# Kernel tuning notes

Measured on AMD Instinct MI355X. Metric: run time of the kernel, lower is better.

The kernel has to match this reference:

```python
import jax, jax.numpy as jnp
import numpy as np

N = 131072
L_ENC = 100
L_DEC = 50
H = 200            # decoder_hidden_dim
SPD = L_ENC + 2 * (L_ENC // 2 + 1)  # 202, signal + amplitudes + phases


def _lin(k, out_d, in_d):
    kw, kb = jax.random.split(k)
    lim = 1.0 / np.sqrt(in_d)
    w = jax.random.uniform(kw, (out_d, in_d), jnp.float32, -lim, lim)
    b = jax.random.uniform(kb, (out_d,), jnp.float32, -lim, lim)
    return w, b


def setup_inputs() -> dict:
    key = jax.random.key(0)
    ks = jax.random.split(key, 16)
    enc_w1, enc_b1 = _lin(ks[0], 100, SPD)
    enc_w2, enc_b2 = _lin(ks[1], SPD, 100)
    enc_wl, enc_bl = _lin(ks[2], H, SPD)
    lim = 1.0 / np.sqrt(H)
    w_ih = jax.random.uniform(ks[3], (3 * H, 1), jnp.float32, -lim, lim)
    w_hh = jax.random.uniform(ks[4], (3 * H, H), jnp.float32, -lim, lim)
    b_ih = jax.random.uniform(ks[5], (3 * H,), jnp.float32, -lim, lim)
    b_hh = jax.random.uniform(ks[6], (3 * H,), jnp.float32, -lim, lim)
    dec_w1, dec_b1 = _lin(ks[7], H // 2, H)
    dec_w2, dec_b2 = _lin(ks[8], H // 4, H // 2)
    dec_w3, dec_b3 = _lin(ks[9], 1, H // 4)
    encoder_input = jax.random.normal(ks[10], (N, L_ENC, 1), jnp.float32)
    return dict(encoder_input=encoder_input,
                enc_w1=enc_w1, enc_b1=enc_b1, enc_w2=enc_w2, enc_b2=enc_b2,
                enc_wl=enc_wl, enc_bl=enc_bl,
                w_ih=w_ih, w_hh=w_hh, b_ih=b_ih, b_hh=b_hh,
                dec_w1=dec_w1, dec_b1=dec_b1, dec_w2=dec_w2, dec_b2=dec_b2,
                dec_w3=dec_w3, dec_b3=dec_b3)


def _lrelu(x):
    return jax.nn.leaky_relu(x, negative_slope=0.01)


def reference(encoder_input, enc_w1, enc_b1, enc_w2, enc_b2, enc_wl, enc_bl,
              w_ih, w_hh, b_ih, b_hh,
              dec_w1, dec_b1, dec_w2, dec_b2, dec_w3, dec_b3):
    # --- MLPEncoder: rfft features + 3-layer MLP ---
    f = jnp.fft.rfft(encoder_input, axis=1, norm='forward')  # [N, 51, 1] complex
    sig = jnp.concatenate([encoder_input, jnp.abs(f), jnp.angle(f)], axis=1)[..., 0]  # [N, 202]
    x = _lrelu(sig @ enc_w1.T + enc_b1)
    x = _lrelu(x @ enc_w2.T + enc_b2)
    h0 = x @ enc_wl.T + enc_bl  # [N, H]

    dec_in0 = encoder_input[:, -1, :]  # [N, 1]

    def step(carry, _):
        h, dec_in = carry
        gx = dec_in @ w_ih.T + b_ih       # [N, 3H]
        gh = h @ w_hh.T + b_hh            # [N, 3H]
        xr, xz, xn = jnp.split(gx, 3, axis=-1)
        hr, hz, hn = jnp.split(gh, 3, axis=-1)
        r = jax.nn.sigmoid(xr + hr)
        z = jax.nn.sigmoid(xz + hz)
        n = jnp.tanh(xn + r * hn)
        h_new = (1.0 - z) * n + z * h
        y = _lrelu(h_new @ dec_w1.T + dec_b1)
        y = _lrelu(y @ dec_w2.T + dec_b2)
        y = y @ dec_w3.T + dec_b3         # [N, 1]
        return (h_new, jax.lax.stop_gradient(y)), y

    _, ys = jax.lax.scan(step, (h0, dec_in0), None, length=L_DEC)  # [L_DEC, N, 1]
    return jnp.transpose(ys, (1, 0, 2))  # [N, L_DEC, 1]
```

## Files before the change

kernel.cpp:

```cpp
#include <hip/hip_runtime.h>
#include <math.h>

typedef _Float16 half8  __attribute__((ext_vector_type(8)));
typedef float    floatx4 __attribute__((ext_vector_type(4)));

#define MFMA16(a, b, c) __builtin_amdgcn_mfma_f32_16x16x32_f16((a), (b), (c), 0, 0, 0)

constexpr unsigned WJT_OFF  = 0;
constexpr unsigned WD1_OFF  = 292864;
constexpr unsigned W2_OFF   = 350208;
constexpr unsigned WE1_OFF  = 366592;
constexpr unsigned WE2_OFF  = 416768;
constexpr unsigned WEL_OFF  = 470016;
constexpr unsigned WIHC_OFF = 563200;
constexpr unsigned BSUM_OFF = 565696;
constexpr unsigned BHHN_OFF = 568192;
constexpr unsigned B1P_OFF  = 569024;
constexpr unsigned B2P_OFF  = 569472;
constexpr unsigned W3P_OFF  = 569728;
constexpr unsigned BE1_OFF  = 569984;
constexpr unsigned BE2_OFF  = 570432;
constexpr unsigned BEL_OFF  = 571264;
constexpr unsigned B3_OFF   = 572096;
constexpr unsigned CT_OFF   = 572112;
constexpr unsigned WS_NEED  = 573712;

constexpr unsigned BST_OFF   = 106496;
constexpr unsigned W2L_OFF   = 129024;
constexpr unsigned CHK_OFF   = 146432;
constexpr unsigned DECIN_OFF = 162816;
constexpr unsigned SMEM_BYTES = 163840;

__device__ __forceinline__ half8 lds_frag16(const _Float16* p) {
  union { uint4 u; half8 h; } cv;
  cv.u = *(const uint4*)p;
  return cv.h;
}
__device__ __forceinline__ half8 g_frag(const _Float16* p) {
  union { uint4 u; half8 h; } cv;
  cv.u = *(const uint4*)p;
  return cv.h;
}
__device__ __forceinline__ void gload_lds16(const _Float16* gsrc, _Float16* lds) {
  __builtin_amdgcn_global_load_lds(
      (const __attribute__((address_space(1))) unsigned int*)gsrc,
      (__attribute__((address_space(3))) unsigned int*)lds, 16, 0, 0);
}
__device__ __forceinline__ float sigm(float x) {
  return __builtin_amdgcn_rcpf(1.f + __builtin_amdgcn_exp2f(-1.44269504f * x));
}
__device__ __forceinline__ float tanh_(float x) {
  return 1.f - 2.f * __builtin_amdgcn_rcpf(1.f + __builtin_amdgcn_exp2f(2.88539008f * x));
}
__device__ __forceinline__ int chk_idx(int row, int col) {
  return (row * 32 + col) ^ (((row >> 1) & 3) << 3);
}

__global__ __launch_bounds__(256) void prep_kernel(
    const float* __restrict__ enc_w1, const float* __restrict__ enc_b1,
    const float* __restrict__ enc_w2, const float* __restrict__ enc_b2,
    const float* __restrict__ enc_wl, const float* __restrict__ enc_bl,
    const float* __restrict__ w_ih,  const float* __restrict__ w_hh,
    const float* __restrict__ b_ih,  const float* __restrict__ b_hh,
    const float* __restrict__ dw1, const float* __restrict__ db1,
    const float* __restrict__ dw2, const float* __restrict__ db2,
    const float* __restrict__ dw3, const float* __restrict__ db3,
    unsigned char* __restrict__ ws)
{
  const int g = blockIdx.x * blockDim.x + threadIdx.x;
  const int st = gridDim.x * blockDim.x;
  _Float16* WJT = (_Float16*)(ws + WJT_OFF);
  for (int i = g; i < 13 * 11264; i += st) {
    int jt = i / 11264, rem = i - jt * 11264;
    int gg = rem / 3712, rem2 = rem - gg * 3712;
    float v = 0.f;
    if (gg < 3) {
      int rr = rem2 / 232, k = rem2 - rr * 232;
      int j = jt * 16 + rr;
      if (j < 200 && k < 200) v = w_hh[(gg * 200 + j) * 200 + k];
    }
    WJT[i] = (_Float16)v;
  }
  _Float16* WD1 = (_Float16*)(ws + WD1_OFF);
  for (int i = g; i < 7 * 4096; i += st) {
    int t = i >> 12, rem = i & 4095;
    float v = 0.f;
    if (rem < 3712) {
      int rr = rem / 232, k = rem - rr * 232;
      int j = t * 16 + rr;
      if (j < 100 && k < 200) v = dw1[j * 200 + k];
    }
    WD1[i] = (_Float16)v;
  }
  _Float16* W2 = (_Float16*)(ws + W2_OFF);
  for (int i = g; i < 64 * 128; i += st) {
    int r = i / 128, k = i - r * 128;
    W2[i] = (_Float16)((r < 50 && k < 100) ? dw2[r * 100 + k] : 0.f);
  }
  _Float16* We1 = (_Float16*)(ws + WE1_OFF);
  for (int i = g; i < 112 * 224; i += st) {
    int r = i / 224, k = i - r * 224;
    We1[i] = (_Float16)((r < 100 && k < 202) ? enc_w1[r * 202 + k] : 0.f);
  }
  _Float16* We2 = (_Float16*)(ws + WE2_OFF);
  for (int i = g; i < 208 * 128; i += st) {
    int r = i / 128, k = i - r * 128;
    We2[i] = (_Float16)((r < 202 && k < 100) ? enc_w2[r * 100 + k] : 0.f);
  }
  _Float16* Wel = (_Float16*)(ws + WEL_OFF);
  for (int i = g; i < 208 * 224; i += st) {
    int r = i / 224, k = i - r * 224;
    Wel[i] = (_Float16)((r < 200 && k < 202) ? enc_wl[r * 202 + k] : 0.f);
  }
  float* wihc = (float*)(ws + WIHC_OFF);
  float* bsum = (float*)(ws + BSUM_OFF);
  for (int i = g; i < 624; i += st) {
    int gg = i / 208, j = i - gg * 208;
    wihc[i] = (j < 200) ? w_ih[gg * 200 + j] : 0.f;
    float b = 0.f;
    if (j < 200) b = (gg < 2) ? (b_ih[gg * 200 + j] + b_hh[gg * 200 + j]) : b_ih[400 + j];
    bsum[i] = b;
  }
  float* bhhn = (float*)(ws + BHHN_OFF);
  for (int i = g; i < 208; i += st) bhhn[i] = (i < 200) ? b_hh[400 + i] : 0.f;
  float* b1p = (float*)(ws + B1P_OFF);
  for (int i = g; i < 112; i += st) b1p[i] = (i < 100) ? db1[i] : 0.f;
  float* b2p = (float*)(ws + B2P_OFF);
  for (int i = g; i < 64; i += st) b2p[i] = (i < 50) ? db2[i] : 0.f;
  float* w3p = (float*)(ws + W3P_OFF);
  for (int i = g; i < 64; i += st) w3p[i] = (i < 50) ? dw3[i] : 0.f;
  float* be1 = (float*)(ws + BE1_OFF);
  for (int i = g; i < 112; i += st) be1[i] = (i < 100) ? enc_b1[i] : 0.f;
  float* be2 = (float*)(ws + BE2_OFF);
  for (int i = g; i < 208; i += st) be2[i] = (i < 202) ? enc_b2[i] : 0.f;
  float* bel = (float*)(ws + BEL_OFF);
  for (int i = g; i < 208; i += st) bel[i] = (i < 200) ? enc_bl[i] : 0.f;
  if (g == 0) *(float*)(ws + B3_OFF) = db3[0];
  double* ct = (double*)(ws + CT_OFF);
  for (int m = g; m < 100; m += st) {
    double c, s;
    if      (m == 0)  { c = 1.0;  s = 0.0; }
    else if (m == 25) { c = 0.0;  s = -1.0; }
    else if (m == 50) { c = -1.0; s = 0.0; }
    else if (m == 75) { c = 0.0;  s = 1.0; }
    else { double a = -2.0 * 3.14159265358979323846 * (double)m / 100.0; c = cos(a); s = sin(a); }
    ct[2 * m]     = c * 0.01;
    ct[2 * m + 1] = s * 0.01;
  }
}

__global__ __launch_bounds__(512, 1) void fused_kernel(
    const float* __restrict__ enc_in, const unsigned char* __restrict__ ws,
    float* __restrict__ out)
{
  __shared__ __align__(16) unsigned char smem[SMEM_BYTES];
  _Float16* Hb    = (_Float16*)smem;
  _Float16* BST   = (_Float16*)(smem + BST_OFF);
  _Float16* W2L   = (_Float16*)(smem + W2L_OFF);
  float*    DECIN = (float*)(smem + DECIN_OFF);
  double*   CTL   = (double*)(smem + CHK_OFF);

  const _Float16* WJTp = (const _Float16*)(ws + WJT_OFF);
  const _Float16* WD1p = (const _Float16*)(ws + WD1_OFF);
  const _Float16* W2w  = (const _Float16*)(ws + W2_OFF);
  const _Float16* We1  = (const _Float16*)(ws + WE1_OFF);
  const _Float16* We2  = (const _Float16*)(ws + WE2_OFF);
  const _Float16* Wel  = (const _Float16*)(ws + WEL_OFF);
  const float* wihc = (const float*)(ws + WIHC_OFF);
  const float* bsum = (const float*)(ws + BSUM_OFF);
  const float* bhhn = (const float*)(ws + BHHN_OFF);
  const float* b1p  = (const float*)(ws + B1P_OFF);
  const float* b2p  = (const float*)(ws + B2P_OFF);
  const float* w3p  = (const float*)(ws + W3P_OFF);
  const float* be1  = (const float*)(ws + BE1_OFF);
  const float* be2  = (const float*)(ws + BE2_OFF);
  const float* bel  = (const float*)(ws + BEL_OFF);
  const float b3v   = *(const float*)(ws + B3_OFF);

  const int tid = threadIdx.x;
  const int lane = tid & 63, wv = tid >> 6;
  const int q = lane >> 4, c = lane & 15;
  const int row0 = blockIdx.x * 256;
  const half8 Z8 = {};

  {
    const double* ctg = (const double*)(ws + CT_OFF);
    for (int i = tid; i < 200; i += 512) CTL[i] = ctg[i];
  }

#pragma unroll 1
  for (int sub = 0; sub < 4; ++sub) {
    float*    XF  = (float*)(smem + sub * 26624);
    _Float16* X1  = (_Float16*)(smem + sub * 26624);
    _Float16* SIG = (_Float16*)(smem + BST_OFF);
    __syncthreads();
    for (int i = tid; i < 6400; i += 512) {
      int r = i / 100, t = i - r * 100;
      XF[r * 101 + t] = enc_in[(size_t)(row0 + sub * 64 + r) * 100 + t];
    }
    for (int i = tid; i < 64 * 6; i += 512) {
      int r = i / 6; SIG[r * 208 + 202 + (i - r * 6)] = (_Float16)0.f;
    }
    __syncthreads();
    for (int kb = wv; kb < 51; kb += 8) {
      double re = 0.0, im = 0.0; int m = 0;
      const float* xr = XF + lane * 101;
      for (int t = 0; t < 100; ++t) {
        double x = (double)xr[t];
        re = fma(x, CTL[2 * m], re);
        im = fma(x, CTL[2 * m + 1], im);
        m += kb; if (m >= 100) m -= 100;
      }
      if (kb == 0 || kb == 50) im = 0.0;
      float ab = (float)sqrt(re * re + im * im);
      float an = atan2f((float)im, (float)re);
      SIG[lane * 208 + 100 + kb] = (_Float16)ab;
      SIG[lane * 208 + 151 + kb] = (_Float16)an;
    }
    for (int i = tid; i < 6400; i += 512) {
      int r = i / 100, t = i - r * 100;
      SIG[r * 208 + t] = (_Float16)XF[r * 101 + t];
    }
    __syncthreads();
#pragma unroll 1
    for (int jt = wv; jt < 7; jt += 8) {
      floatx4 C[4] = {{0,0,0,0},{0,0,0,0},{0,0,0,0},{0,0,0,0}};
      const _Float16* wp = We1 + (jt * 16 + c) * 224 + q * 8;
#pragma unroll
      for (int s = 0; s < 7; ++s) {
        half8 B = g_frag(wp + s * 32);
#pragma unroll
        for (int m = 0; m < 4; ++m) {
          half8 Af = (s == 6 && q >= 2) ? Z8 : lds_frag16(SIG + (m * 16 + c) * 208 + q * 8 + s * 32);
          C[m] = MFMA16(Af, B, C[m]);
        }
      }
      int col = jt * 16 + c; float bv = be1[col]; bool wm = col < 104;
#pragma unroll
      for (int m = 0; m < 4; ++m)
#pragma unroll
        for (int r = 0; r < 4; ++r) {
          float v = C[m][r] + bv; v = fmaxf(v, 0.01f * v);
          if (wm) X1[(m * 16 + 4 * q + r) * 104 + col] = (_Float16)v;
        }
    }
    __syncthreads();
#pragma unroll 1
    for (int jt = wv; jt < 13; jt += 8) {
      floatx4 C[4] = {{0,0,0,0},{0,0,0,0},{0,0,0,0},{0,0,0,0}};
      const _Float16* wp = We2 + (jt * 16 + c) * 128 + q * 8;
#pragma unroll
      for (int s = 0; s < 4; ++s) {
        half8 B = g_frag(wp + s * 32);
#pragma unroll
        for (int m = 0; m < 4; ++m) {
          half8 Af = (s == 3 && q >= 1) ? Z8 : lds_frag16(X1 + (m * 16 + c) * 104 + q * 8 + s * 32);
          C[m] = MFMA16(Af, B, C[m]);
        }
      }
      int col = jt * 16 + c; float bv = be2[col];
#pragma unroll
      for (int m = 0; m < 4; ++m)
#pragma unroll
        for (int r = 0; r < 4; ++r) {
          float v = C[m][r] + bv; v = fmaxf(v, 0.01f * v);
          SIG[(m * 16 + 4 * q + r) * 208 + col] = (_Float16)v;
        }
    }
    __syncthreads();
#pragma unroll 1
    for (int jt = wv; jt < 13; jt += 8) {
      floatx4 C[4] = {{0,0,0,0},{0,0,0,0},{0,0,0,0},{0,0,0,0}};
      const _Float16* wp = Wel + (jt * 16 + c) * 224 + q * 8;
#pragma unroll
      for (int s = 0; s < 7; ++s) {
        half8 B = g_frag(wp + s * 32);
#pragma unroll
        for (int m = 0; m < 4; ++m) {
          half8 Af = (s == 6 && q >= 2) ? Z8 : lds_frag16(SIG + (m * 16 + c) * 208 + q * 8 + s * 32);
          C[m] = MFMA16(Af, B, C[m]);
        }
      }
      int col = jt * 16 + c; float bv = bel[col]; bool wm = col < 200;
#pragma unroll
      for (int m = 0; m < 4; ++m)
#pragma unroll
        for (int r = 0; r < 4; ++r) {
          float v = C[m][r] + bv;
          if (wm) Hb[(sub * 64 + m * 16 + 4 * q + r) * 208 + col] = (_Float16)v;
        }
    }
  }
  __syncthreads();
  for (int i = tid; i < 256 * 8; i += 512) {
    int r = i / 8; Hb[r * 208 + 200 + (i - r * 8)] = (_Float16)0.f;
  }
  for (int i = tid; i < 256; i += 512)
    DECIN[i] = enc_in[(size_t)(row0 + i) * 100 + 99];
  for (int i = tid; i < 1024; i += 512) {
    int r = i / 16, kc = i - r * 16;
    *(uint4*)(W2L + r * 136 + kc * 8) = *(const uint4*)(W2w + r * 128 + kc * 8);
  }
  __syncthreads();

  _Float16* myH   = Hb + wv * 32 * 208;
  _Float16* myCHK = (_Float16*)(smem + CHK_OFF) + wv * 1024;

#pragma unroll 1
  for (int k = 0; k <= 50; ++k) {
    half8 A[2][7];
#pragma unroll
    for (int m = 0; m < 2; ++m)
#pragma unroll
      for (int s = 0; s < 7; ++s)
        A[m][s] = (s == 6 && q >= 2) ? Z8 : lds_frag16(myH + (m * 16 + c) * 208 + s * 32 + q * 8);

    if (k >= 1) {
      half8 A2[2][4];
#pragma unroll
      for (int jtp = 0; jtp < 4; ++jtp) {
        const int njt = (jtp == 3) ? 1 : 2;
        __syncthreads();
        for (int i = wv; i < njt * 8; i += 8) {
          int jj = i >> 3, p = i & 7;
          gload_lds16(WD1p + (jtp * 2 + jj) * 4096 + p * 512 + lane * 8,
                      BST + jj * 4096 + p * 512);
        }
        __syncthreads();
#pragma unroll
        for (int jj = 0; jj < 2; ++jj) {
          if (jj < njt) {
            floatx4 C[2] = {{0,0,0,0},{0,0,0,0}};
#pragma unroll
            for (int s = 0; s < 7; ++s) {
              half8 B = lds_frag16(BST + jj * 4096 + c * 232 + s * 32 + q * 8);
#pragma unroll
              for (int m = 0; m < 2; ++m) C[m] = MFMA16(A[m][s], B, C[m]);
            }
            int col = (jtp * 2 + jj) * 16 + c; float bv = b1p[col];
#pragma unroll
            for (int m = 0; m < 2; ++m)
#pragma unroll
              for (int r = 0; r < 4; ++r) {
                float v = C[m][r] + bv; v = fmaxf(v, 0.01f * v);
                myCHK[chk_idx(m * 16 + 4 * q + r, jj * 16 + c)] = (_Float16)v;
              }
          }
        }
#pragma unroll
        for (int m = 0; m < 2; ++m)
          A2[m][jtp] = (jtp == 3 && q >= 2) ? Z8 : lds_frag16(myCHK + chk_idx(m * 16 + c, q * 8));
      }
      float ya[2][4] = {{0,0,0,0},{0,0,0,0}};
#pragma unroll
      for (int jt2 = 0; jt2 < 4; ++jt2) {
        floatx4 Cy[2] = {{0,0,0,0},{0,0,0,0}};
#pragma unroll
        for (int s2 = 0; s2 < 4; ++s2) {
          half8 B = lds_frag16(W2L + (jt2 * 16 + c) * 136 + s2 * 32 + q * 8);
#pragma unroll
          for (int m = 0; m < 2; ++m) Cy[m] = MFMA16(A2[m][s2], B, Cy[m]);
        }
        int col2 = jt2 * 16 + c; float b2v = b2p[col2], w3v = w3p[col2];
#pragma unroll
        for (int m = 0; m < 2; ++m)
#pragma unroll
          for (int r = 0; r < 4; ++r) {
            float v = Cy[m][r] + b2v; v = fmaxf(v, 0.01f * v);
            ya[m][r] = fmaf(v, w3v, ya[m][r]);
          }
      }
#pragma unroll
      for (int m = 0; m < 2; ++m)
#pragma unroll
        for (int r = 0; r < 4; ++r) {
          float v = ya[m][r];
          v += __shfl_xor(v, 1); v += __shfl_xor(v, 2);
          v += __shfl_xor(v, 4); v += __shfl_xor(v, 8);
          if (c == 0) {
            int rowL = wv * 32 + m * 16 + 4 * q + r;
            float y = v + b3v;
            DECIN[rowL] = y;
            out[(size_t)(row0 + rowL) * 50 + (k - 1)] = y;
          }
        }
    }
    if (k <= 49) {
      float dreg[8];
#pragma unroll
      for (int m = 0; m < 2; ++m)
#pragma unroll
        for (int r = 0; r < 4; ++r)
          dreg[m * 4 + r] = DECIN[wv * 32 + m * 16 + 4 * q + r];
#pragma unroll 1
      for (int jt = 0; jt < 13; ++jt) {
        __syncthreads();
        for (int i = wv; i < 22; i += 8) {
          gload_lds16(WJTp + jt * 11264 + i * 512 + lane * 8,
                      BST + i * 512);
        }
        __syncthreads();
        floatx4 Cr[2] = {{0,0,0,0},{0,0,0,0}};
        floatx4 Cz[2] = {{0,0,0,0},{0,0,0,0}};
        floatx4 Cn[2] = {{0,0,0,0},{0,0,0,0}};
#pragma unroll
        for (int s = 0; s < 7; ++s) {
          half8 Br = lds_frag16(BST + c * 232 + s * 32 + q * 8);
          half8 Bz = lds_frag16(BST + 3712 + c * 232 + s * 32 + q * 8);
          half8 Bn = lds_frag16(BST + 7424 + c * 232 + s * 32 + q * 8);
#pragma unroll
          for (int m = 0; m < 2; ++m) {
            Cr[m] = MFMA16(A[m][s], Br, Cr[m]);
            Cz[m] = MFMA16(A[m][s], Bz, Cz[m]);
            Cn[m] = MFMA16(A[m][s], Bn, Cn[m]);
          }
        }
        int col = jt * 16 + c;
        float wr = wihc[col], wz = wihc[208 + col], wn = wihc[416 + col];
        float br = bsum[col], bz = bsum[208 + col], bnih = bsum[416 + col];
        float bnhh = bhhn[col];
        bool wm = col < 200;
#pragma unroll
        for (int m = 0; m < 2; ++m) {
          _Float16* hp = myH + (m * 16 + 4 * q) * 208 + col;
#pragma unroll
          for (int r = 0; r < 4; ++r) {
            float d  = dreg[m * 4 + r];
            float ho = (float)hp[r * 208];
            float rgate = sigm(Cr[m][r] + fmaf(d, wr, br));
            float zgate = sigm(Cz[m][r] + fmaf(d, wz, bz));
            float ngate = tanh_(fmaf(d, wn, bnih) + rgate * (Cn[m][r] + bnhh));
            float hv = fmaf(zgate, ho - ngate, ngate);
            if (wm) hp[r * 208] = (_Float16)hv;
          }
        }
      }
    }
  }
}

extern "C" void kernel_launch(void* const* d_in, const int* in_sizes, int n_in,
                              void* d_out, int out_size, void* d_ws, size_t ws_size,
                              hipStream_t stream) {
  const float* enc_in = (const float*)d_in[0];
  const float* enc_w1 = (const float*)d_in[1];
  const float* enc_b1 = (const float*)d_in[2];
  const float* enc_w2 = (const float*)d_in[3];
  const float* enc_b2 = (const float*)d_in[4];
  const float* enc_wl = (const float*)d_in[5];
  const float* enc_bl = (const float*)d_in[6];
  const float* w_ih   = (const float*)d_in[7];
  const float* w_hh   = (const float*)d_in[8];
  const float* b_ih   = (const float*)d_in[9];
  const float* b_hh   = (const float*)d_in[10];
  const float* dw1    = (const float*)d_in[11];
  const float* db1    = (const float*)d_in[12];
  const float* dw2    = (const float*)d_in[13];
  const float* db2    = (const float*)d_in[14];
  const float* dw3    = (const float*)d_in[15];
  const float* db3    = (const float*)d_in[16];
  unsigned char* ws = (unsigned char*)d_ws;
  float* out = (float*)d_out;

  prep_kernel<<<dim3(256), dim3(256), 0, stream>>>(
      enc_w1, enc_b1, enc_w2, enc_b2, enc_wl, enc_bl,
      w_ih, w_hh, b_ih, b_hh, dw1, db1, dw2, db2, dw3, db3, ws);
  fused_kernel<<<dim3(512), dim3(512), 0, stream>>>(enc_in, ws, out);
}
```

Measured before the change: 3.445 ms.

## Double-buffer GRU and decoder weight tiles in LDS, keep hidden state in registers

The GRU recurrent and decoder first-layer weight tiles are now double-buffered in LDS. The next tile's global-to-LDS load is issued before computing on the current one, which removes one barrier per tile and overlaps weight streaming with the MFMA work. Weight padding shrinks from a row stride of 232 to 216, with zero fragments substituted for the padded K tail, and LDS is relaid out to hold both buffers. The hidden state is also kept in registers for the old-h read, and a row swizzle is added to the H buffer layout to reduce bank conflicts. The cost is more register pressure from the 13x2 half4 hidden array and full unrolling of the jt loop.

```diff
diff --git a/kernel.cpp b/kernel.cpp
--- a/kernel.cpp
+++ b/kernel.cpp
@@ -2,34 +2,37 @@
 #include <math.h>
 
 typedef _Float16 half8  __attribute__((ext_vector_type(8)));
+typedef _Float16 half4  __attribute__((ext_vector_type(4)));
 typedef float    floatx4 __attribute__((ext_vector_type(4)));
 
 #define MFMA16(a, b, c) __builtin_amdgcn_mfma_f32_16x16x32_f16((a), (b), (c), 0, 0, 0)
 
 constexpr unsigned WJT_OFF  = 0;
-constexpr unsigned WD1_OFF  = 292864;
-constexpr unsigned W2_OFF   = 350208;
-constexpr unsigned WE1_OFF  = 366592;
-constexpr unsigned WE2_OFF  = 416768;
-constexpr unsigned WEL_OFF  = 470016;
-constexpr unsigned WIHC_OFF = 563200;
-constexpr unsigned BSUM_OFF = 565696;
-constexpr unsigned BHHN_OFF = 568192;
-constexpr unsigned B1P_OFF  = 569024;
-constexpr unsigned B2P_OFF  = 569472;
-constexpr unsigned W3P_OFF  = 569728;
-constexpr unsigned BE1_OFF  = 569984;
-constexpr unsigned BE2_OFF  = 570432;
-constexpr unsigned BEL_OFF  = 571264;
-constexpr unsigned B3_OFF   = 572096;
-constexpr unsigned CT_OFF   = 572112;
-constexpr unsigned WS_NEED  = 573712;
-
-constexpr unsigned BST_OFF   = 106496;
-constexpr unsigned W2L_OFF   = 129024;
-constexpr unsigned CHK_OFF   = 146432;
-constexpr unsigned DECIN_OFF = 162816;
-constexpr unsigned SMEM_BYTES = 163840;
+constexpr unsigned WD1_OFF  = 269568;
+constexpr unsigned W2_OFF   = 319744;
+constexpr unsigned WE1_OFF  = 336128;
+constexpr unsigned WE2_OFF  = 386304;
+constexpr unsigned WEL_OFF  = 439552;
+constexpr unsigned WIHC_OFF = 532736;
+constexpr unsigned BSUM_OFF = 535232;
+constexpr unsigned BHHN_OFF = 537728;
+constexpr unsigned B1P_OFF  = 538560;
+constexpr unsigned B2P_OFF  = 539008;
+constexpr unsigned W3P_OFF  = 539264;
+constexpr unsigned BE1_OFF  = 539520;
+constexpr unsigned BE2_OFF  = 539968;
+constexpr unsigned BEL_OFF  = 540800;
+constexpr unsigned B3_OFF   = 541632;
+constexpr unsigned CT_OFF   = 541648;
+
+constexpr unsigned RG_OFF    = 106496;
+constexpr unsigned GB1_OFF   = 127232;
+constexpr unsigned WB1_OFF   = 113664;
+constexpr unsigned CHK_OFF   = 120832;
+constexpr unsigned CTL_OFF   = 133120;
+constexpr unsigned W2L_OFF   = 147968;
+constexpr unsigned DECIN_OFF = 162112;
+constexpr unsigned SMEM_BYTES = 163136;
 
 __device__ __forceinline__ half8 lds_frag16(const _Float16* p) {
   union { uint4 u; half8 h; } cv;
@@ -51,6 +54,9 @@
 }
 __device__ __forceinline__ float tanh_(float x) {
   return 1.f - 2.f * __builtin_amdgcn_rcpf(1.f + __builtin_amdgcn_exp2f(2.88539008f * x));
+}
+__device__ __forceinline__ int hb_idx(int row, int col) {
+  return (row * 208 + col) ^ (((row >> 2) & 1) << 3);
 }
 __device__ __forceinline__ int chk_idx(int row, int col) {
   return (row * 32 + col) ^ (((row >> 1) & 3) << 3);
@@ -70,25 +76,21 @@
   const int g = blockIdx.x * blockDim.x + threadIdx.x;
   const int st = gridDim.x * blockDim.x;
   _Float16* WJT = (_Float16*)(ws + WJT_OFF);
-  for (int i = g; i < 13 * 11264; i += st) {
-    int jt = i / 11264, rem = i - jt * 11264;
-    int gg = rem / 3712, rem2 = rem - gg * 3712;
+  for (int i = g; i < 13 * 10368; i += st) {
+    int jt = i / 10368, rem = i - jt * 10368;
+    int gg = rem / 3456, rem2 = rem - gg * 3456;
+    int rr = rem2 / 216, kk = rem2 - rr * 216;
+    int j = jt * 16 + rr;
+    WJT[i] = (_Float16)((j < 200 && kk < 200) ? w_hh[(gg * 200 + j) * 200 + kk] : 0.f);
+  }
+  _Float16* WD1 = (_Float16*)(ws + WD1_OFF);
+  for (int i = g; i < 7 * 3584; i += st) {
+    int t = i / 3584, rem = i - t * 3584;
     float v = 0.f;
-    if (gg < 3) {
-      int rr = rem2 / 232, k = rem2 - rr * 232;
-      int j = jt * 16 + rr;
-      if (j < 200 && k < 200) v = w_hh[(gg * 200 + j) * 200 + k];
-    }
-    WJT[i] = (_Float16)v;
-  }
-  _Float16* WD1 = (_Float16*)(ws + WD1_OFF);
-  for (int i = g; i < 7 * 4096; i += st) {
-    int t = i >> 12, rem = i & 4095;
-    float v = 0.f;
-    if (rem < 3712) {
-      int rr = rem / 232, k = rem - rr * 232;
+    if (rem < 3456) {
+      int rr = rem / 216, kk = rem - rr * 216;
       int j = t * 16 + rr;
-      if (j < 100 && k < 200) v = dw1[j * 200 + k];
+      if (j < 100 && kk < 200) v = dw1[j * 200 + kk];
     }
     WD1[i] = (_Float16)v;
   }
@@ -155,10 +157,13 @@
 {
   __shared__ __align__(16) unsigned char smem[SMEM_BYTES];
   _Float16* Hb    = (_Float16*)smem;
-  _Float16* BST   = (_Float16*)(smem + BST_OFF);
+  _Float16* GB0   = (_Float16*)(smem + RG_OFF);
+  _Float16* GB1   = (_Float16*)(smem + GB1_OFF);
+  _Float16* WB0   = (_Float16*)(smem + RG_OFF);
+  _Float16* WB1   = (_Float16*)(smem + WB1_OFF);
   _Float16* W2L   = (_Float16*)(smem + W2L_OFF);
   float*    DECIN = (float*)(smem + DECIN_OFF);
-  double*   CTL   = (double*)(smem + CHK_OFF);
+  double*   CTL   = (double*)(smem + CTL_OFF);
 
   const _Float16* WJTp = (const _Float16*)(ws + WJT_OFF);
   const _Float16* WD1p = (const _Float16*)(ws + WD1_OFF);
@@ -192,7 +197,7 @@
   for (int sub = 0; sub < 4; ++sub) {
     float*    XF  = (float*)(smem + sub * 26624);
     _Float16* X1  = (_Float16*)(smem + sub * 26624);
-    _Float16* SIG = (_Float16*)(smem + BST_OFF);
+    _Float16* SIG = (_Float16*)(smem + RG_OFF);
     __syncthreads();
     for (int i = tid; i < 6400; i += 512) {
       int r = i / 100, t = i - r * 100;
@@ -287,23 +292,31 @@
 #pragma unroll
         for (int r = 0; r < 4; ++r) {
           float v = C[m][r] + bv;
-          if (wm) Hb[(sub * 64 + m * 16 + 4 * q + r) * 208 + col] = (_Float16)v;
+          if (wm) Hb[hb_idx(sub * 64 + m * 16 + 4 * q + r, col)] = (_Float16)v;
         }
     }
   }
   __syncthreads();
   for (int i = tid; i < 256 * 8; i += 512) {
-    int r = i / 8; Hb[r * 208 + 200 + (i - r * 8)] = (_Float16)0.f;
+    int r = i >> 3; Hb[hb_idx(r, 200 + (i & 7))] = (_Float16)0.f;
   }
   for (int i = tid; i < 256; i += 512)
     DECIN[i] = enc_in[(size_t)(row0 + i) * 100 + 99];
-  for (int i = tid; i < 1024; i += 512) {
-    int r = i / 16, kc = i - r * 16;
+  for (int i = tid; i < 832; i += 512) {
+    int r = i >> 4, kc = i & 15;
     *(uint4*)(W2L + r * 136 + kc * 8) = *(const uint4*)(W2w + r * 128 + kc * 8);
   }
   __syncthreads();
 
-  _Float16* myH   = Hb + wv * 32 * 208;
+  half4 hreg[13][2];
+#pragma unroll
+  for (int jt = 0; jt < 13; ++jt)
+#pragma unroll
+    for (int m = 0; m < 2; ++m)
+#pragma unroll
+      for (int r = 0; r < 4; ++r)
+        hreg[jt][m][r] = Hb[hb_idx(wv * 32 + m * 16 + 4 * q + r, jt * 16 + c)];
+
   _Float16* myCHK = (_Float16*)(smem + CHK_OFF) + wv * 1024;
 
 #pragma unroll 1
@@ -313,43 +326,47 @@
     for (int m = 0; m < 2; ++m)
 #pragma unroll
       for (int s = 0; s < 7; ++s)
-        A[m][s] = (s == 6 && q >= 2) ? Z8 : lds_frag16(myH + (m * 16 + c) * 208 + s * 32 + q * 8);
+        A[m][s] = (s == 6 && q >= 2) ? Z8 : lds_frag16(Hb + hb_idx(wv * 32 + m * 16 + c, s * 32 + q * 8));
 
     if (k >= 1) {
       half8 A2[2][4];
-#pragma unroll
-      for (int jtp = 0; jtp < 4; ++jtp) {
-        const int njt = (jtp == 3) ? 1 : 2;
+      __syncthreads();
+      for (int i = wv; i < 7; i += 8)
+        gload_lds16(WD1p + i * 512 + lane * 8, WB0 + i * 512);
+#pragma unroll
+      for (int t = 0; t < 7; ++t) {
         __syncthreads();
-        for (int i = wv; i < njt * 8; i += 8) {
-          int jj = i >> 3, p = i & 7;
-          gload_lds16(WD1p + (jtp * 2 + jj) * 4096 + p * 512 + lane * 8,
-                      BST + jj * 4096 + p * 512);
-        }
-        __syncthreads();
-#pragma unroll
-        for (int jj = 0; jj < 2; ++jj) {
-          if (jj < njt) {
-            floatx4 C[2] = {{0,0,0,0},{0,0,0,0}};
-#pragma unroll
-            for (int s = 0; s < 7; ++s) {
-              half8 B = lds_frag16(BST + jj * 4096 + c * 232 + s * 32 + q * 8);
-#pragma unroll
-              for (int m = 0; m < 2; ++m) C[m] = MFMA16(A[m][s], B, C[m]);
-            }
-            int col = (jtp * 2 + jj) * 16 + c; float bv = b1p[col];
-#pragma unroll
-            for (int m = 0; m < 2; ++m)
-#pragma unroll
-              for (int r = 0; r < 4; ++r) {
-                float v = C[m][r] + bv; v = fmaxf(v, 0.01f * v);
-                myCHK[chk_idx(m * 16 + 4 * q + r, jj * 16 + c)] = (_Float16)v;
-              }
-          }
-        }
+        if (t < 6) {
+          _Float16* dst = ((t + 1) & 1) ? WB1 : WB0;
+          for (int i = wv; i < 7; i += 8)
+            gload_lds16(WD1p + (t + 1) * 3584 + i * 512 + lane * 8, dst + i * 512);
+        }
+        const _Float16* wb_ = (t & 1) ? WB1 : WB0;
+        floatx4 C[2] = {{0,0,0,0},{0,0,0,0}};
+#pragma unroll
+        for (int s = 0; s < 7; ++s) {
+          half8 B = (s == 6 && q >= 2) ? Z8 : lds_frag16(wb_ + c * 216 + s * 32 + q * 8);
+#pragma unroll
+          for (int m = 0; m < 2; ++m) C[m] = MFMA16(A[m][s], B, C[m]);
+        }
+        int col = t * 16 + c; float bv = b1p[col];
 #pragma unroll
         for (int m = 0; m < 2; ++m)
-          A2[m][jtp] = (jtp == 3 && q >= 2) ? Z8 : lds_frag16(myCHK + chk_idx(m * 16 + c, q * 8));
+#pragma unroll
+          for (int r = 0; r < 4; ++r) {
+            float v = C[m][r] + bv; v = fmaxf(v, 0.01f * v);
+            myCHK[chk_idx(m * 16 + 4 * q + r, (t & 1) * 16 + c)] = (_Float16)v;
+          }
+        if (t & 1) {
+#pragma unroll
+          for (int m = 0; m < 2; ++m)
+            A2[m][t >> 1] = lds_frag16(myCHK + chk_idx(m * 16 + c, q * 8));
+        }
+        if (t == 6) {
+#pragma unroll
+          for (int m = 0; m < 2; ++m)
+            A2[m][3] = (q >= 2) ? Z8 : lds_frag16(myCHK + chk_idx(m * 16 + c, q * 8));
+        }
       }
       float ya[2][4] = {{0,0,0,0},{0,0,0,0}};
 #pragma unroll
@@ -357,7 +374,7 @@
         floatx4 Cy[2] = {{0,0,0,0},{0,0,0,0}};
 #pragma unroll
         for (int s2 = 0; s2 < 4; ++s2) {
-          half8 B = lds_frag16(W2L + (jt2 * 16 + c) * 136 + s2 * 32 + q * 8);
+          half8 B = (jt2 == 3 && c >= 4) ? Z8 : lds_frag16(W2L + (jt2 * 16 + c) * 136 + s2 * 32 + q * 8);
 #pragma unroll
           for (int m = 0; m < 2; ++m) Cy[m] = MFMA16(A2[m][s2], B, Cy[m]);
         }
@@ -392,22 +409,31 @@
 #pragma unroll
         for (int r = 0; r < 4; ++r)
           dreg[m * 4 + r] = DECIN[wv * 32 + m * 16 + 4 * q + r];
-#pragma unroll 1
+      __syncthreads();
+      for (int i = wv; i < 21; i += 8) {
+        if (i < 20 || lane < 16)
+          gload_lds16(WJTp + i * 512 + lane * 8, GB0 + i * 512);
+      }
+#pragma unroll
       for (int jt = 0; jt < 13; ++jt) {
         __syncthreads();
-        for (int i = wv; i < 22; i += 8) {
-          gload_lds16(WJTp + jt * 11264 + i * 512 + lane * 8,
-                      BST + i * 512);
-        }
-        __syncthreads();
+        if (jt < 12) {
+          _Float16* dst = ((jt + 1) & 1) ? GB1 : GB0;
+          for (int i = wv; i < 21; i += 8) {
+            if (i < 20 || lane < 16)
+              gload_lds16(WJTp + (jt + 1) * 10368 + i * 512 + lane * 8, dst + i * 512);
+          }
+        }
+        const _Float16* buf = (jt & 1) ? GB1 : GB0;
         floatx4 Cr[2] = {{0,0,0,0},{0,0,0,0}};
         floatx4 Cz[2] = {{0,0,0,0},{0,0,0,0}};
         floatx4 Cn[2] = {{0,0,0,0},{0,0,0,0}};
 #pragma unroll
         for (int s = 0; s < 7; ++s) {
-          half8 Br = lds_frag16(BST + c * 232 + s * 32 + q * 8);
-          half8 Bz = lds_frag16(BST + 3712 + c * 232 + s * 32 + q * 8);
-          half8 Bn = lds_frag16(BST + 7424 + c * 232 + s * 32 + q * 8);
+          bool bm = (s == 6) && (q >= 2);
+          half8 Br = bm ? Z8 : lds_frag16(buf + c * 216 + s * 32 + q * 8);
+          half8 Bz = bm ? Z8 : lds_frag16(buf + 3456 + c * 216 + s * 32 + q * 8);
+          half8 Bn = bm ? Z8 : lds_frag16(buf + 6912 + c * 216 + s * 32 + q * 8);
 #pragma unroll
           for (int m = 0; m < 2; ++m) {
             Cr[m] = MFMA16(A[m][s], Br, Cr[m]);
@@ -422,16 +448,17 @@
         bool wm = col < 200;
 #pragma unroll
         for (int m = 0; m < 2; ++m) {
-          _Float16* hp = myH + (m * 16 + 4 * q) * 208 + col;
 #pragma unroll
           for (int r = 0; r < 4; ++r) {
             float d  = dreg[m * 4 + r];
-            float ho = (float)hp[r * 208];
+            float ho = (float)hreg[jt][m][r];
             float rgate = sigm(Cr[m][r] + fmaf(d, wr, br));
             float zgate = sigm(Cz[m][r] + fmaf(d, wz, bz));
             float ngate = tanh_(fmaf(d, wn, bnih) + rgate * (Cn[m][r] + bnhh));
             float hv = fmaf(zgate, ho - ngate, ngate);
-            if (wm) hp[r * 208] = (_Float16)hv;
+            _Float16 hh = (_Float16)hv;
+            hreg[jt][m][r] = hh;
+            if (wm) Hb[hb_idx(wv * 32 + m * 16 + 4 * q + r, col)] = hh;
           }
         }
       }
```

New measurement: 11.57 ms. 236% more time.
